# Kernel optimization log

Measured on AMD Instinct MI355X. Metric: run time of the kernel, lower is better.

## Reference

```python
import jax, jax.numpy as jnp
import numpy as np

D_MODEL = 512
D_STATE = 16
D_INNER = 2 * D_MODEL  # expand_factor=2
IN_CH = 256
B_SZ, H_SZ, W_SZ = 4, 32, 32


def setup_inputs() -> dict:
    key = jax.random.key(0)
    ks = jax.random.split(key, 24)
    f = jax.random.normal
    inp = {}
    inp["x_V"] = f(ks[0], (B_SZ, IN_CH, H_SZ, W_SZ), jnp.float32)
    inp["x_I"] = f(ks[1], (B_SZ, IN_CH, H_SZ, W_SZ), jnp.float32)
    # channel_reduce: 1x1 conv + BN (inference stats)
    inp["conv_red_w"] = f(ks[2], (D_MODEL, IN_CH), jnp.float32) * 0.05
    inp["bn_red_g"] = jnp.ones((D_MODEL,), jnp.float32)
    inp["bn_red_b"] = jnp.zeros((D_MODEL,), jnp.float32)
    inp["bn_red_m"] = jnp.zeros((D_MODEL,), jnp.float32)
    inp["bn_red_v"] = jnp.ones((D_MODEL,), jnp.float32)
    # channel_restore: 1x1 conv + BN
    inp["conv_res_w"] = f(ks[3], (IN_CH, D_MODEL), jnp.float32) * 0.05
    inp["bn_res_g"] = jnp.ones((IN_CH,), jnp.float32)
    inp["bn_res_b"] = jnp.zeros((IN_CH,), jnp.float32)
    inp["bn_res_m"] = jnp.zeros((IN_CH,), jnp.float32)
    inp["bn_res_v"] = jnp.ones((IN_CH,), jnp.float32)
    # lambda_predictor convs (1x1 on pooled features == linear)
    inp["lam_w1"] = f(ks[4], (D_MODEL // 4, D_MODEL * 2), jnp.float32) * 0.05
    inp["lam_b1"] = jnp.zeros((D_MODEL // 4,), jnp.float32)
    inp["lam_w2"] = f(ks[5], (2, D_MODEL // 4), jnp.float32) * 0.05
    inp["lam_b2"] = jnp.zeros((2,), jnp.float32)
    # two SimplifiedMamba2Blocks
    for i, p in enumerate(["V", "I"]):
        kk = jax.random.split(ks[6 + i], 6)
        inp[p + "_in_w"] = f(kk[0], (2 * D_INNER, D_MODEL), jnp.float32) * 0.03
        inp[p + "_out_w"] = f(kk[1], (D_MODEL, D_INNER), jnp.float32) * 0.03
        # A = -exp(A_log) in (-1, -0.05): stable decay
        inp[p + "_A_log"] = jnp.log(jax.random.uniform(kk[2], (D_INNER, D_STATE), jnp.float32, 0.05, 0.95))
        inp[p + "_B"] = f(kk[3], (D_INNER, D_STATE), jnp.float32) * 0.05
        inp[p + "_C"] = jnp.full((D_INNER, D_STATE), 0.01, jnp.float32)
        inp[p + "_ln_g"] = jnp.ones((D_MODEL,), jnp.float32)
        inp[p + "_ln_b"] = jnp.zeros((D_MODEL,), jnp.float32)
    inp["gate"] = jnp.asarray(0.1, jnp.float32)
    return inp


def _bn(x, g, b, m, v):
    # x: (B,C,H,W); inference-mode batchnorm
    return (x - m[:, None, None]) / jnp.sqrt(v[:, None, None] + 1e-5) * g[:, None, None] + b[:, None, None]


def _conv1x1(x, w):
    return jnp.einsum('bchw,oc->bohw', x, w)


def _ssm_scan(x_ssm, A, Bm, Cm, reverse):
    # x_ssm: (B,L,I); A,Bm,Cm: (I,S)
    bsz = x_ssm.shape[0]
    h0 = jnp.zeros((bsz, A.shape[0], A.shape[1]), x_ssm.dtype)

    def step(h, xt):  # xt: (B,I)
        h = jnp.clip(h * A + xt[:, :, None] * Bm, -10.0, 10.0)
        return h, jnp.einsum('bis,is->bi', h, Cm)

    _, ys = jax.lax.scan(step, h0, jnp.swapaxes(x_ssm, 0, 1), reverse=reverse)
    return jnp.swapaxes(ys, 0, 1)  # (B,L,I), in original time order


def _mamba(x, ln_g, ln_b, in_w, out_w, A_log, Bm, Cm):
    # LayerNorm
    mu = jnp.mean(x, -1, keepdims=True)
    var = jnp.mean((x - mu) ** 2, -1, keepdims=True)
    xn = (x - mu) / jnp.sqrt(var + 1e-5) * ln_g + ln_b
    xp = xn @ in_w.T  # (B,L,2*I)
    x_ssm, gate = jnp.split(xp, 2, axis=-1)
    A = jnp.clip(-jnp.exp(A_log), -10.0, -0.01)
    yf = _ssm_scan(x_ssm, A, Bm, Cm, False)
    yb = _ssm_scan(x_ssm, A, Bm, Cm, True)
    out = 0.5 * (yf + yb) * jax.nn.silu(gate)
    return out @ out_w.T


def reference(x_V, x_I, conv_red_w, bn_red_g, bn_red_b, bn_red_m, bn_red_v,
              conv_res_w, bn_res_g, bn_res_b, bn_res_m, bn_res_v,
              lam_w1, lam_b1, lam_w2, lam_b2,
              V_in_w, V_out_w, V_A_log, V_B, V_C, V_ln_g, V_ln_b,
              I_in_w, I_out_w, I_A_log, I_B, I_C, I_ln_g, I_ln_b, gate):
    B, _, H, W = x_V.shape
    xVr = jax.nn.relu(_bn(_conv1x1(x_V, conv_red_w), bn_red_g, bn_red_b, bn_red_m, bn_red_v))
    xIr = jax.nn.relu(_bn(_conv1x1(x_I, conv_red_w), bn_red_g, bn_red_b, bn_red_m, bn_red_v))
    # same spatial size -> adaptive pooling and [:B] slicing are identities
    conc = jnp.concatenate([xVr, xIr], axis=1)  # (B, 2*d_model, H, W)

    def lam(c):
        p = jnp.mean(c, axis=(2, 3))  # global avg pool -> (B, 2*d_model)
        h1 = jax.nn.relu(p @ lam_w1.T + lam_b1)
        return jax.nn.softmax(h1 @ lam_w2.T + lam_b2, axis=-1)  # (B,2)

    lamV = lam(conc)
    lamI = lam(conc)

    seq_V = jnp.swapaxes(xVr.reshape(B, D_MODEL, H * W), 1, 2)  # (B,L,D)
    seq_I = jnp.swapaxes(xIr.reshape(B, D_MODEL, H * W), 1, 2)

    outV_std = _mamba(seq_V, V_ln_g, V_ln_b, V_in_w, V_out_w, V_A_log, V_B, V_C)
    outI_std = _mamba(seq_I, I_ln_g, I_ln_b, I_in_w, I_out_w, I_A_log, I_B, I_C)
    outV_cross = _mamba(seq_V, V_ln_g, V_ln_b, V_in_w, V_out_w, V_A_log, jax.lax.stop_gradient(I_B), V_C)
    outI_cross = _mamba(seq_I, I_ln_g, I_ln_b, I_in_w, I_out_w, I_A_log, jax.lax.stop_gradient(V_B), I_C)

    outV = lamV[:, 0][:, None, None] * outV_std + lamV[:, 1][:, None, None] * outV_cross
    outI = lamI[:, 0][:, None, None] * outI_std + lamI[:, 1][:, None, None] * outI_cross

    featV = jnp.swapaxes(outV, 1, 2).reshape(B, D_MODEL, H, W)
    featI = jnp.swapaxes(outI, 1, 2).reshape(B, D_MODEL, H, W)
    featV = _bn(_conv1x1(featV, conv_res_w), bn_res_g, bn_res_b, bn_res_m, bn_res_v)
    featI = _bn(_conv1x1(featI, conv_res_w), bn_res_g, bn_res_b, bn_res_m, bn_res_v)

    g = jax.nn.sigmoid(gate)
    return (x_V + g * featV, x_I + g * featI)
```

## Files before the change

### kernel.cpp

```cpp
#include <hip/hip_runtime.h>
#include <hip/hip_bf16.h>
#include <math.h>

#define L_SZ 1024
#define DM   512
#define DI   1024
#define NS   16
#define CH   256

typedef float4 f4;
typedef __attribute__((ext_vector_type(8))) short short8;
typedef __attribute__((ext_vector_type(8))) unsigned short u16x8;
typedef __attribute__((ext_vector_type(4))) float f32x4;

__device__ __forceinline__ float bf2f(ushort u) {
    union { unsigned int i; float f; } x; x.i = ((unsigned int)u) << 16; return x.f;
}
__device__ __forceinline__ ushort f2bf(float f) {
    union { float f; unsigned int i; } x; x.f = f;
    unsigned int r = x.i + 0x7FFFu + ((x.i >> 16) & 1u);
    return (ushort)(r >> 16);
}
__device__ __forceinline__ uint pkbf(float a, float b) {
    union { __hip_bfloat162 h; uint u; } c;
    c.h = __float22bfloat162_rn(make_float2(a, b));
    return c.u;
}

#define GLOAD16(gp, lp) \
  __builtin_amdgcn_global_load_lds((const __attribute__((address_space(1))) void*)(gp), \
                                   (__attribute__((address_space(3))) void*)(lp), 16, 0, 0)

__global__ __launch_bounds__(256) void k_prep(
    const float* __restrict__ s0, const float* __restrict__ s1,
    const float* __restrict__ s2, const float* __restrict__ s3,
    const float* __restrict__ s4, const float* __restrict__ s5,
    ushort* __restrict__ d0, ushort* __restrict__ d1,
    ushort* __restrict__ d2, ushort* __restrict__ d3,
    ushort* __restrict__ d4, ushort* __restrict__ d5,
    const float* __restrict__ xv, const float* __restrict__ xi,
    ushort* __restrict__ xtv, ushort* __restrict__ xti,
    float* __restrict__ p, unsigned int* __restrict__ cnt)
{
    __shared__ float tile[32][36];
    const int bid = blockIdx.x;
    const int t = threadIdx.x;
    if (bid < 3328) {
        const float* s; ushort* d; int rel;
        if      (bid < 128)  { s = s0; d = d0; rel = bid; }
        else if (bid < 256)  { s = s1; d = d1; rel = bid - 128; }
        else if (bid < 1280) { s = s2; d = d2; rel = bid - 256; }
        else if (bid < 2304) { s = s3; d = d3; rel = bid - 1280; }
        else if (bid < 2816) { s = s4; d = d4; rel = bid - 2304; }
        else                 { s = s5; d = d5; rel = bid - 2816; }
        const int i = rel * 256 + t;
        f4 v = ((const f4*)s)[i];
        ushort4 o;
        o.x = f2bf(v.x); o.y = f2bf(v.y); o.z = f2bf(v.z); o.w = f2bf(v.w);
        ((ushort4*)d)[i] = o;
        return;
    }
    if (bid < 5376) {
        const int rel = bid - 3328;
        const int l0 = (rel & 31) * 32, c0 = ((rel >> 5) & 7) * 32;
        const int z = rel >> 8;
        const int b = z & 3, st = z >> 2;
        const float* x = st ? xi : xv;
        ushort* xt = st ? xti : xtv;
        {
            int cc = t >> 3, ll4 = (t & 7) << 2;
            f4 v = *(const f4*)(x + ((size_t)(b * CH + c0 + cc)) * L_SZ + l0 + ll4);
            tile[cc][ll4 + 0] = v.x; tile[cc][ll4 + 1] = v.y;
            tile[cc][ll4 + 2] = v.z; tile[cc][ll4 + 3] = v.w;
        }
        __syncthreads();
        {
            int ll = t >> 3, cc4 = (t & 7) << 2;
            ushort4 o;
            o.x = f2bf(tile[cc4 + 0][ll]); o.y = f2bf(tile[cc4 + 1][ll]);
            o.z = f2bf(tile[cc4 + 2][ll]); o.w = f2bf(tile[cc4 + 3][ll]);
            *(ushort4*)(xt + ((size_t)(b * L_SZ + l0 + ll)) * CH + c0 + cc4) = o;
        }
        return;
    }
    const f4 z4 = {0.f, 0.f, 0.f, 0.f};
    ((f4*)p)[t]       = z4;
    ((f4*)p)[t + 256] = z4;
    ((f4*)p)[t + 512] = z4;
    ((f4*)p)[t + 768] = z4;
    if (t == 0) *cnt = 0u;
}

template<int MODE, int BM, int BN>
__global__ __launch_bounds__(256) void k_gemm(
    const ushort* __restrict__ A0, const ushort* __restrict__ A1,
    const ushort* __restrict__ B0, const ushort* __restrict__ B1,
    int K,
    float* __restrict__ o0, float* __restrict__ o1,
    ushort* __restrict__ ob0, ushort* __restrict__ ob1,
    ushort* __restrict__ sb0, ushort* __restrict__ sb1,
    const float* __restrict__ pg, const float* __restrict__ pb,
    const float* __restrict__ pm, const float* __restrict__ pv,
    const float* __restrict__ x0, const float* __restrict__ x1,
    const float* __restrict__ gate, float* __restrict__ pp)
{
    constexpr int MT   = BM / 32;
    constexpr int NT   = BN / 32;
    constexpr int ASEG = BM / 16;
    constexpr int NSEG = (BM + BN) / 16;
    constexpr int SPW  = NSEG / 4;
    __shared__ __align__(16) ushort Sl[(BM + BN) * 32];
    const int t = threadIdx.x;
    const int wv = t >> 6, lane = t & 63;
    const int n0 = blockIdx.x * BN, m0 = blockIdx.y * BM;
    const int st = blockIdx.z;
    const ushort* Ap = st ? A1 : A0;
    const ushort* Bp = st ? B1 : B0;
    const int wm = wv >> 1, wn = wv & 1;
    const int lrow = lane & 15, q = lane >> 4;
    f32x4 acc[MT][NT];
    #pragma unroll
    for (int a_ = 0; a_ < MT; ++a_)
        #pragma unroll
        for (int b_ = 0; b_ < NT; ++b_)
            acc[a_][b_] = (f32x4){0.f, 0.f, 0.f, 0.f};
    const int srow = lane >> 2;
    const int skk  = (((lane & 3) ^ ((lane >> 3) & 3)) << 3);
    const int koff = ((q ^ ((lrow >> 1) & 3)) << 3);
    for (int k0 = 0; k0 < K; k0 += 32) {
        #pragma unroll
        for (int s2 = 0; s2 < SPW; ++s2) {
            const int seg = wv * SPW + s2;
            const int grow = (seg < ASEG) ? (m0 + seg * 16 + srow)
                                          : (n0 + (seg - ASEG) * 16 + srow);
            const ushort* src = (seg < ASEG) ? Ap : Bp;
            GLOAD16(src + (size_t)grow * K + k0 + skk, &Sl[seg * 512]);
        }
        __syncthreads();
        short8 af[MT], bfr[NT];
        #pragma unroll
        for (int mt = 0; mt < MT; ++mt)
            af[mt] = *(const short8*)&Sl[(wm * (MT * 16) + mt * 16 + lrow) * 32 + koff];
        #pragma unroll
        for (int nt = 0; nt < NT; ++nt)
            bfr[nt] = *(const short8*)&Sl[(BM + wn * (NT * 16) + nt * 16 + lrow) * 32 + koff];
        #pragma unroll
        for (int mt = 0; mt < MT; ++mt)
            #pragma unroll
            for (int nt = 0; nt < NT; ++nt)
                acc[mt][nt] = __builtin_amdgcn_mfma_f32_16x16x32_bf16(af[mt], bfr[nt], acc[mt][nt], 0, 0, 0);
        __syncthreads();
    }
    if (MODE == 0) {
        ushort* sq = st ? ob1 : ob0;
        const int b = m0 >> 10;
        #pragma unroll
        for (int nt = 0; nt < NT; ++nt) {
            const int gn = n0 + wn * (NT * 16) + nt * 16 + lrow;
            const float s  = pg[gn] * rsqrtf(pv[gn] + 1e-5f);
            const float sh = pb[gn] - pm[gn] * s;
            float psum = 0.f;
            #pragma unroll
            for (int mt = 0; mt < MT; ++mt) {
                const int gm = m0 + wm * (MT * 16) + mt * 16 + q * 4;
                float v[4];
                #pragma unroll
                for (int r = 0; r < 4; ++r) {
                    v[r] = fmaxf(fmaf(acc[mt][nt][r], s, sh), 0.f);
                    psum += v[r];
                }
                const uint u01 = pkbf(v[0], v[1]);
                const uint u23 = pkbf(v[2], v[3]);
                ushort* bp = sq + (size_t)gm * DM + gn;
                bp[0]      = (ushort)u01;
                bp[DM]     = (ushort)(u01 >> 16);
                bp[2 * DM] = (ushort)u23;
                bp[3 * DM] = (ushort)(u23 >> 16);
            }
            psum += __shfl_xor(psum, 16, 64);
            psum += __shfl_xor(psum, 32, 64);
            if (q == 0)
                atomicAdd(pp + (b * 1024 + st * 512 + gn), psum * (1.0f / 1024.0f));
        }
    } else if (MODE == 1) {
        const bool isx = (n0 < 1024);
        ushort* xp = st ? ob1 : ob0;
        ushort* sp = st ? sb1 : sb0;
        #pragma unroll
        for (int nt = 0; nt < NT; ++nt) {
            const int gn = n0 + wn * (NT * 16) + nt * 16 + lrow;
            #pragma unroll
            for (int mt = 0; mt < MT; ++mt) {
                const int gm = m0 + wm * (MT * 16) + mt * 16 + q * 4;
                if (isx) {
                    const uint u01 = pkbf(acc[mt][nt][0], acc[mt][nt][1]);
                    const uint u23 = pkbf(acc[mt][nt][2], acc[mt][nt][3]);
                    ushort* bp = xp + (size_t)gm * DI + gn;
                    bp[0]      = (ushort)u01;
                    bp[DI]     = (ushort)(u01 >> 16);
                    bp[2 * DI] = (ushort)u23;
                    bp[3 * DI] = (ushort)(u23 >> 16);
                } else {
                    float sv[4];
                    #pragma unroll
                    for (int r = 0; r < 4; ++r) {
                        const float v = acc[mt][nt][r];
                        sv[r] = v / (1.f + __expf(-v));
                    }
                    const uint u01 = pkbf(sv[0], sv[1]);
                    const uint u23 = pkbf(sv[2], sv[3]);
                    ushort* bp = sp + (size_t)gm * DI + gn - 1024;
                    bp[0]      = (ushort)u01;
                    bp[DI]     = (ushort)(u01 >> 16);
                    bp[2 * DI] = (ushort)u23;
                    bp[3 * DI] = (ushort)(u23 >> 16);
                }
            }
        }
    } else if (MODE == 2) {
        ushort* fp_ = st ? ob1 : ob0;
        #pragma unroll
        for (int nt = 0; nt < NT; ++nt) {
            const int gn = n0 + wn * (NT * 16) + nt * 16 + lrow;
            #pragma unroll
            for (int mt = 0; mt < MT; ++mt) {
                const int gm = m0 + wm * (MT * 16) + mt * 16 + q * 4;
                const uint u01 = pkbf(acc[mt][nt][0], acc[mt][nt][1]);
                const uint u23 = pkbf(acc[mt][nt][2], acc[mt][nt][3]);
                ushort* bp = fp_ + (size_t)gm * DM + gn;
                bp[0]      = (ushort)u01;
                bp[DM]     = (ushort)(u01 >> 16);
                bp[2 * DM] = (ushort)u23;
                bp[3 * DM] = (ushort)(u23 >> 16);
            }
        }
    } else {
        const float* xin = st ? x1 : x0;
        float* op = st ? o1 : o0;
        const float g = 1.f / (1.f + __expf(-gate[0]));
        #pragma unroll
        for (int nt = 0; nt < NT; ++nt) {
            const int gn = n0 + wn * (NT * 16) + nt * 16 + lrow;
            const float s  = pg[gn] * rsqrtf(pv[gn] + 1e-5f);
            const float sh = pb[gn] - pm[gn] * s;
            #pragma unroll
            for (int mt = 0; mt < MT; ++mt) {
                const int gmb = m0 + wm * (MT * 16) + mt * 16 + q * 4;
                const int b = gmb >> 10, l = gmb & 1023;
                const size_t off = ((size_t)(b * CH + gn)) * L_SZ + l;
                f4 xi = *(const f4*)(xin + off);
                f4 o;
                o.x = xi.x + g * fmaf(acc[mt][nt][0], s, sh);
                o.y = xi.y + g * fmaf(acc[mt][nt][1], s, sh);
                o.z = xi.z + g * fmaf(acc[mt][nt][2], s, sh);
                o.w = xi.w + g * fmaf(acc[mt][nt][3], s, sh);
                *(f4*)(op + off) = o;
            }
        }
    }
}

__global__ __launch_bounds__(256) void k_lam(
    const float* __restrict__ p, const float* __restrict__ w1,
    const float* __restrict__ b1, const float* __restrict__ w2,
    const float* __restrict__ b2, float* __restrict__ h1,
    float* __restrict__ lam, unsigned int* __restrict__ cnt)
{
    __shared__ float lsm[8];
    __shared__ unsigned int tick;
    const int t = threadIdx.x, lane = t & 63, wv = t >> 6;
    const int idx = blockIdx.x * 4 + wv;
    const int b = idx >> 7, j = idx & 127;
    const float* pb = p + b * 1024;
    const float* wr = w1 + j * 1024;
    float s = 0.f;
    #pragma unroll
    for (int k = 0; k < 16; ++k)
        s = fmaf(pb[lane + k * 64], wr[lane + k * 64], s);
    #pragma unroll
    for (int off = 1; off < 64; off <<= 1) s += __shfl_xor(s, off, 64);
    if (lane == 0) h1[idx] = fmaxf(s + b1[j], 0.f);
    __threadfence();
    __syncthreads();
    if (t == 0) tick = atomicAdd(cnt, 1u);
    __syncthreads();
    if (tick != 127u) return;
    __threadfence();
    {
        const int g32 = t >> 5, l32 = t & 31;
        const int bb = g32 >> 1, kk = g32 & 1;
        const float* hb = h1 + bb * 128;
        const float* wr2 = w2 + kk * 128;
        float ss = 0.f;
        #pragma unroll
        for (int u = 0; u < 4; ++u)
            ss = fmaf(hb[l32 + u * 32], wr2[l32 + u * 32], ss);
        #pragma unroll
        for (int off = 1; off < 32; off <<= 1) ss += __shfl_xor(ss, off, 64);
        if (l32 == 0) lsm[g32] = ss + b2[kk];
    }
    __syncthreads();
    if (t < 4) {
        const float a0 = lsm[t * 2], a1 = lsm[t * 2 + 1];
        const float m  = fmaxf(a0, a1);
        const float e0 = __expf(a0 - m), e1 = __expf(a1 - m);
        const float inv = 1.f / (e0 + e1);
        lam[t * 2 + 0] = e0 * inv;
        lam[t * 2 + 1] = e1 * inv;
    }
}

__global__ __launch_bounds__(256) void k_ln(
    const ushort* __restrict__ seq0, const ushort* __restrict__ seq1,
    const float* __restrict__ g0, const float* __restrict__ b0,
    const float* __restrict__ g1, const float* __restrict__ b1,
    ushort* __restrict__ ln0, ushort* __restrict__ ln1)
{
    const int t = threadIdx.x, lane = t & 63, wv = t >> 6;
    const int row = blockIdx.x * 4 + wv, st = blockIdx.y;
    const ushort* seq = st ? seq1 : seq0;
    const float* gg  = st ? g1 : g0;
    const float* bb  = st ? b1 : b0;
    ushort* ln = st ? ln1 : ln0;
    const u16x8 v = *(const u16x8*)(seq + (size_t)row * DM + lane * 8);
    float f[8];
    float s = 0.f, ss = 0.f;
    #pragma unroll
    for (int i = 0; i < 8; ++i) {
        f[i] = bf2f(v[i]);
        s += f[i];
        ss = fmaf(f[i], f[i], ss);
    }
    #pragma unroll
    for (int off = 1; off < 64; off <<= 1) {
        s += __shfl_xor(s, off, 64); ss += __shfl_xor(ss, off, 64);
    }
    const float mu = s * (1.f / 512.f);
    const float rstd = rsqrtf(ss * (1.f / 512.f) - mu * mu + 1e-5f);
    const f4 gv0 = *(const f4*)(gg + lane * 8);
    const f4 gv1 = *(const f4*)(gg + lane * 8 + 4);
    const f4 bv0 = *(const f4*)(bb + lane * 8);
    const f4 bv1 = *(const f4*)(bb + lane * 8 + 4);
    const float gvv[8] = {gv0.x, gv0.y, gv0.z, gv0.w, gv1.x, gv1.y, gv1.z, gv1.w};
    const float bvv[8] = {bv0.x, bv0.y, bv0.z, bv0.w, bv1.x, bv1.y, bv1.z, bv1.w};
    u16x8 o;
    #pragma unroll
    for (int i = 0; i < 8; i += 2) {
        const uint u = pkbf(fmaf((f[i]     - mu) * rstd, gvv[i],     bvv[i]),
                            fmaf((f[i + 1] - mu) * rstd, gvv[i + 1], bvv[i + 1]));
        o[i]     = (ushort)u;
        o[i + 1] = (ushort)(u >> 16);
    }
    *(u16x8*)(ln + (size_t)row * DM + lane * 8) = o;
}

__global__ __launch_bounds__(256) void k_scan(
    const ushort* __restrict__ xsV, const ushort* __restrict__ xsI,
    const float* __restrict__ VA, const float* __restrict__ VB,
    const float* __restrict__ VC, const float* __restrict__ IA,
    const float* __restrict__ IB, const float* __restrict__ IC,
    const float* __restrict__ lam,
    ushort* __restrict__ accfV, ushort* __restrict__ accbV,
    ushort* __restrict__ accfI, ushort* __restrict__ accbI)
{
    __shared__ __align__(16) ushort xbuf[2][32][128];
    const int t = threadIdx.x;
    const int lane = t & 63, wv = t >> 6;
    const int shalf = t & 1;
    const int il = t >> 1;
    const int b = blockIdx.y;
    const int cfg = blockIdx.z & 3, j = blockIdx.z >> 2;
    const int st = cfg >> 1, dir = cfg & 1;
    const ushort* xs = st ? xsI : xsV;
    const float* Alog = st ? IA : VA;
    const float* Cm   = st ? IC : VC;
    const float* Bown = st ? IB : VB;
    const float* Both = st ? VB : IB;
    ushort* out = st ? (dir ? accbI : accfI) : (dir ? accbV : accfV);
    const float lam0 = lam[b * 2 + 0], lam1 = lam[b * 2 + 1];
    float a[8], w[8], g[8];
    const int base = (blockIdx.x * 128 + il) * NS + shalf * 8;
    #pragma unroll
    for (int s = 0; s < 8; ++s) {
        a[s] = fminf(fmaxf(-__expf(Alog[base + s]), -10.f), -0.01f);
        w[s] = 0.5f * Cm[base + s] * fmaf(lam0, Bown[base + s], lam1 * Both[base + s]);
        g[s] = 0.f;
    }
    const ushort* xbase = xs + (size_t)b * L_SZ * DI + blockIdx.x * 128;
    ushort* op = out + (size_t)b * L_SZ * DI + blockIdx.x * 128 + il;
    const int c0    = j == 0 ? 0 : 4 * j - 3;
    const int ncha  = j == 0 ? 4 : 7;
    const int nwarm = j == 0 ? 0 : 3;
    const int lrow  = wv * 4 + (lane >> 4);
    const int lcol8 = (lane & 15) << 3;
    {
        #pragma unroll
        for (int is = 0; is < 2; ++is) {
            const int lr = (c0 << 5) + is * 16 + lrow;
            const int l  = dir ? (1023 - lr) : lr;
            GLOAD16(xbase + (size_t)l * DI + lcol8, &xbuf[0][is * 16 + wv * 4][0]);
        }
    }
    __syncthreads();
    for (int ci = 0; ci < ncha; ++ci) {
        const int cidx = c0 + ci;
        const int buf = ci & 1;
        if (ci + 1 < ncha) {
            #pragma unroll
            for (int is = 0; is < 2; ++is) {
                const int lr = ((cidx + 1) << 5) + is * 16 + lrow;
                const int l  = dir ? (1023 - lr) : lr;
                GLOAD16(xbase + (size_t)l * DI + lcol8, &xbuf[buf ^ 1][is * 16 + wv * 4][0]);
            }
        }
        if (ci < nwarm) {
            #pragma unroll
            for (int n = 0; n < 32; ++n) {
                const float x = bf2f(xbuf[buf][n][il]);
                #pragma unroll
                for (int s = 0; s < 8; ++s)
                    g[s] = fmaf(a[s], g[s], x);
            }
        } else {
            #pragma unroll
            for (int n = 0; n < 32; ++n) {
                const float x = bf2f(xbuf[buf][n][il]);
                float y0 = 0.f, y1 = 0.f;
                #pragma unroll
                for (int s = 0; s < 8; s += 2) {
                    g[s]     = fmaf(a[s],     g[s],     x);
                    y0       = fmaf(g[s],     w[s],     y0);
                    g[s + 1] = fmaf(a[s + 1], g[s + 1], x);
                    y1       = fmaf(g[s + 1], w[s + 1], y1);
                }
                float z = y0 + y1;
                z += __shfl_xor(z, 1, 64);
                if (shalf == 0) {
                    const int lp = (cidx << 5) + n;
                    const int l  = dir ? (1023 - lp) : lp;
                    op[(size_t)l * DI] = f2bf(z);
                }
            }
        }
        __syncthreads();
    }
}

__global__ __launch_bounds__(256) void k_combine(
    const ushort* __restrict__ fV, const ushort* __restrict__ bV,
    const ushort* __restrict__ fI, const ushort* __restrict__ bI,
    const ushort* __restrict__ sgV, const ushort* __restrict__ sgI,
    ushort* __restrict__ yV, ushort* __restrict__ yI)
{
    const int st = blockIdx.y;
    const size_t i = (size_t)blockIdx.x * 256 + threadIdx.x;
    const ushort4 f = ((const ushort4*)(st ? fI : fV))[i];
    const ushort4 g = ((const ushort4*)(st ? bI : bV))[i];
    const ushort4 s = ((const ushort4*)(st ? sgI : sgV))[i];
    ushort4 o;
    o.x = f2bf((bf2f(f.x) + bf2f(g.x)) * bf2f(s.x));
    o.y = f2bf((bf2f(f.y) + bf2f(g.y)) * bf2f(s.y));
    o.z = f2bf((bf2f(f.z) + bf2f(g.z)) * bf2f(s.z));
    o.w = f2bf((bf2f(f.w) + bf2f(g.w)) * bf2f(s.w));
    ((ushort4*)(st ? yI : yV))[i] = o;
}

extern "C" void kernel_launch(void* const* d_in, const int* in_sizes, int n_in,
                              void* d_out, int out_size, void* d_ws, size_t ws_size,
                              hipStream_t stream)
{
    const float* xV       = (const float*)d_in[0];
    const float* xI       = (const float*)d_in[1];
    const float* convredw = (const float*)d_in[2];
    const float* bnredg   = (const float*)d_in[3];
    const float* bnredb   = (const float*)d_in[4];
    const float* bnredm   = (const float*)d_in[5];
    const float* bnredv   = (const float*)d_in[6];
    const float* convresw = (const float*)d_in[7];
    const float* bnresg   = (const float*)d_in[8];
    const float* bnresb   = (const float*)d_in[9];
    const float* bnresm   = (const float*)d_in[10];
    const float* bnresv   = (const float*)d_in[11];
    const float* lamw1    = (const float*)d_in[12];
    const float* lamb1    = (const float*)d_in[13];
    const float* lamw2    = (const float*)d_in[14];
    const float* lamb2    = (const float*)d_in[15];
    const float* Vinw     = (const float*)d_in[16];
    const float* Voutw    = (const float*)d_in[17];
    const float* VAlog    = (const float*)d_in[18];
    const float* VB       = (const float*)d_in[19];
    const float* VC       = (const float*)d_in[20];
    const float* Vlng     = (const float*)d_in[21];
    const float* Vlnb     = (const float*)d_in[22];
    const float* Iinw     = (const float*)d_in[23];
    const float* Ioutw    = (const float*)d_in[24];
    const float* IAlog    = (const float*)d_in[25];
    const float* IB       = (const float*)d_in[26];
    const float* IC       = (const float*)d_in[27];
    const float* Ilng     = (const float*)d_in[28];
    const float* Ilnb     = (const float*)d_in[29];
    const float* gate     = (const float*)d_in[30];

    char* W = (char*)d_ws;
    const size_t MB = 1048576;
    ushort* seqV  = (ushort*)(W + 0);
    ushort* seqI  = (ushort*)(W + 4  * MB);
    float*  p     = (float*)(W + 8 * MB);
    float*  lam   = (float*)(W + 8 * MB + 16384);
    float*  h1    = (float*)(W + 8 * MB + 32768);
    unsigned int* cnt = (unsigned int*)(W + 8 * MB + 49152);
    ushort* sgV   = (ushort*)(W + 17 * MB);
    ushort* sgI   = (ushort*)(W + 25 * MB);
    ushort* accfV = (ushort*)(W + 33 * MB);
    ushort* accbV = (ushort*)(W + 41 * MB);
    ushort* accfI = (ushort*)(W + 49 * MB);
    ushort* accbI = (ushort*)(W + 57 * MB);
    ushort* wred  = (ushort*)(W + 65 * MB);
    ushort* wres  = (ushort*)(W + 65 * MB + 262144);
    ushort* winV  = (ushort*)(W + 66 * MB);
    ushort* winI  = (ushort*)(W + 68 * MB);
    ushort* woutV = (ushort*)(W + 70 * MB);
    ushort* woutI = (ushort*)(W + 71 * MB);
    ushort* xtV   = (ushort*)(W + 72 * MB);
    ushort* xtI   = (ushort*)(W + 74 * MB);
    ushort* lnV   = (ushort*)(W + 76 * MB);
    ushort* lnI   = (ushort*)(W + 80 * MB);
    ushort* xsV   = (ushort*)(W + 84 * MB);
    ushort* xsI   = (ushort*)(W + 92 * MB);
    ushort* yV    = xsV;
    ushort* yI    = xsI;
    ushort* featV = seqV;
    ushort* featI = seqI;
    float*  outp  = (float*)d_out;

    k_prep<<<dim3(5377), 256, 0, stream>>>(
        convredw, convresw, Vinw, Iinw, Voutw, Ioutw,
        wred, wres, winV, winI, woutV, woutI,
        xV, xI, xtV, xtI, p, cnt);
    k_gemm<0, 128, 64><<<dim3(8, 32, 2), 256, 0, stream>>>(xtV, xtI, wred, wred, 256,
        nullptr, nullptr, seqV, seqI, nullptr, nullptr,
        bnredg, bnredb, bnredm, bnredv, nullptr, nullptr, nullptr, p);
    k_lam<<<128, 256, 0, stream>>>(p, lamw1, lamb1, lamw2, lamb2, h1, lam, cnt);
    k_ln<<<dim3(1024, 2), 256, 0, stream>>>(seqV, seqI, Vlng, Vlnb, Ilng, Ilnb, lnV, lnI);
    k_gemm<1, 128, 128><<<dim3(16, 32, 2), 256, 0, stream>>>(lnV, lnI, winV, winI, 512,
        nullptr, nullptr, xsV, xsI, sgV, sgI,
        nullptr, nullptr, nullptr, nullptr, nullptr, nullptr, nullptr, nullptr);
    k_scan<<<dim3(8, 4, 32), 256, 0, stream>>>(xsV, xsI, VAlog, VB, VC,
        IAlog, IB, IC, lam, accfV, accbV, accfI, accbI);
    k_combine<<<dim3(4096, 2), 256, 0, stream>>>(accfV, accbV, accfI, accbI,
        sgV, sgI, yV, yI);
    k_gemm<2, 128, 64><<<dim3(8, 32, 2), 256, 0, stream>>>(yV, yI, woutV, woutI, 1024,
        nullptr, nullptr, featV, featI, nullptr, nullptr,
        nullptr, nullptr, nullptr, nullptr, nullptr, nullptr, nullptr, nullptr);
    k_gemm<3, 64, 64><<<dim3(4, 64, 2), 256, 0, stream>>>(featV, featI, wres, wres, 512,
        outp, outp + 1048576, nullptr, nullptr, nullptr, nullptr,
        bnresg, bnresb, bnresm, bnresv, xV, xI, gate, nullptr);
}
```

Before: 268.1 us.

## Fuse forward/backward scans and gating combine into a single scan kernel

Each scan block now runs the forward and backward recurrences together over a 128-row window with 64-row warm-up halos. It exchanges the partial outputs through shared memory and applies the silu-gate multiply directly, which removes the separate combine kernel and the four bf16 accumulator buffers. This cuts global traffic and one launch, and it halves the block count while doubling per-thread work and shared memory (about 64KB per block), which may reduce occupancy. The final writes are scalar strided stores plus gate loads per element.

```diff
diff --git a/kernel.cpp b/kernel.cpp
--- a/kernel.cpp
+++ b/kernel.cpp
@@ -356,113 +356,133 @@
 
 __global__ __launch_bounds__(256) void k_scan(
     const ushort* __restrict__ xsV, const ushort* __restrict__ xsI,
+    const ushort* __restrict__ sgV, const ushort* __restrict__ sgI,
     const float* __restrict__ VA, const float* __restrict__ VB,
     const float* __restrict__ VC, const float* __restrict__ IA,
     const float* __restrict__ IB, const float* __restrict__ IC,
     const float* __restrict__ lam,
-    ushort* __restrict__ accfV, ushort* __restrict__ accbV,
-    ushort* __restrict__ accfI, ushort* __restrict__ accbI)
+    ushort* __restrict__ yV, ushort* __restrict__ yI)
 {
-    __shared__ __align__(16) ushort xbuf[2][32][128];
+    __shared__ __align__(16) ushort xf[2][32][128];
+    __shared__ __align__(16) ushort xb[2][32][128];
+    __shared__ ushort yfb[64][128];
+    __shared__ ushort ybb[64][128];
     const int t = threadIdx.x;
     const int lane = t & 63, wv = t >> 6;
     const int shalf = t & 1;
     const int il = t >> 1;
     const int b = blockIdx.y;
-    const int cfg = blockIdx.z & 3, j = blockIdx.z >> 2;
-    const int st = cfg >> 1, dir = cfg & 1;
-    const ushort* xs = st ? xsI : xsV;
+    const int st = blockIdx.z >> 3, j = blockIdx.z & 7;
+    const ushort* xrow  = (st ? xsI : xsV) + (size_t)b * L_SZ * DI + blockIdx.x * 128;
+    const ushort* sgrow = (st ? sgI : sgV) + (size_t)b * L_SZ * DI + blockIdx.x * 128;
+    ushort* yrow        = (st ? yI  : yV ) + (size_t)b * L_SZ * DI + blockIdx.x * 128;
     const float* Alog = st ? IA : VA;
     const float* Cm   = st ? IC : VC;
     const float* Bown = st ? IB : VB;
     const float* Both = st ? VB : IB;
-    ushort* out = st ? (dir ? accbI : accfI) : (dir ? accbV : accfV);
     const float lam0 = lam[b * 2 + 0], lam1 = lam[b * 2 + 1];
-    float a[8], w[8], g[8];
+    float a[8], w[8], gf[8], gb[8];
     const int base = (blockIdx.x * 128 + il) * NS + shalf * 8;
     #pragma unroll
     for (int s = 0; s < 8; ++s) {
         a[s] = fminf(fmaxf(-__expf(Alog[base + s]), -10.f), -0.01f);
         w[s] = 0.5f * Cm[base + s] * fmaf(lam0, Bown[base + s], lam1 * Both[base + s]);
-        g[s] = 0.f;
-    }
-    const ushort* xbase = xs + (size_t)b * L_SZ * DI + blockIdx.x * 128;
-    ushort* op = out + (size_t)b * L_SZ * DI + blockIdx.x * 128 + il;
-    const int c0    = j == 0 ? 0 : 4 * j - 3;
-    const int ncha  = j == 0 ? 4 : 7;
-    const int nwarm = j == 0 ? 0 : 3;
-    const int lrow  = wv * 4 + (lane >> 4);
-    const int lcol8 = (lane & 15) << 3;
-    {
-        #pragma unroll
-        for (int is = 0; is < 2; ++is) {
-            const int lr = (c0 << 5) + is * 16 + lrow;
-            const int l  = dir ? (1023 - lr) : lr;
-            GLOAD16(xbase + (size_t)l * DI + lcol8, &xbuf[0][is * 16 + wv * 4][0]);
-        }
+        gf[s] = 0.f; gb[s] = 0.f;
+    }
+    const int row0 = j << 7;
+    const int lr16 = wv * 4 + (lane >> 4);
+    const int lc8  = (lane & 15) << 3;
+    #pragma unroll
+    for (int is = 0; is < 2; ++is) {
+        const int idx = is * 16 + lr16;
+        int rf = row0 - 64 + idx;
+        rf = max(0, min(1023, rf));
+        GLOAD16(xrow + (size_t)rf * DI + lc8, &xf[0][is * 16 + wv * 4][0]);
+        int rb = row0 + 191 - idx;
+        rb = max(0, min(1023, rb));
+        GLOAD16(xrow + (size_t)rb * DI + lc8, &xb[0][is * 16 + wv * 4][0]);
     }
     __syncthreads();
-    for (int ci = 0; ci < ncha; ++ci) {
-        const int cidx = c0 + ci;
-        const int buf = ci & 1;
-        if (ci + 1 < ncha) {
+    for (int si = 0; si < 6; ++si) {
+        const int buf = si & 1;
+        if (si < 5) {
             #pragma unroll
             for (int is = 0; is < 2; ++is) {
-                const int lr = ((cidx + 1) << 5) + is * 16 + lrow;
-                const int l  = dir ? (1023 - lr) : lr;
-                GLOAD16(xbase + (size_t)l * DI + lcol8, &xbuf[buf ^ 1][is * 16 + wv * 4][0]);
-            }
-        }
-        if (ci < nwarm) {
+                const int idx = is * 16 + lr16;
+                int rf = row0 - 64 + (si + 1) * 32 + idx;
+                rf = max(0, min(1023, rf));
+                GLOAD16(xrow + (size_t)rf * DI + lc8, &xf[buf ^ 1][is * 16 + wv * 4][0]);
+                int rb = row0 + 191 - (si + 1) * 32 - idx;
+                rb = max(0, min(1023, rb));
+                GLOAD16(xrow + (size_t)rb * DI + lc8, &xb[buf ^ 1][is * 16 + wv * 4][0]);
+            }
+        }
+        if (si == 2) {
+            if (j == 0) for (int s = 0; s < 8; ++s) gf[s] = 0.f;
+            if (j == 7) for (int s = 0; s < 8; ++s) gb[s] = 0.f;
+        }
+        if (si < 2) {
             #pragma unroll
             for (int n = 0; n < 32; ++n) {
-                const float x = bf2f(xbuf[buf][n][il]);
+                const float vf = bf2f(xf[buf][n][il]);
+                const float vb = bf2f(xb[buf][n][il]);
                 #pragma unroll
-                for (int s = 0; s < 8; ++s)
-                    g[s] = fmaf(a[s], g[s], x);
+                for (int s = 0; s < 8; ++s) {
+                    gf[s] = fmaf(a[s], gf[s], vf);
+                    gb[s] = fmaf(a[s], gb[s], vb);
+                }
+            }
+        } else if (si < 4) {
+            const int nb = (si - 2) * 32;
+            #pragma unroll
+            for (int n = 0; n < 32; ++n) {
+                const float vf = bf2f(xf[buf][n][il]);
+                const float vb = bf2f(xb[buf][n][il]);
+                float yf = 0.f, yb = 0.f;
+                #pragma unroll
+                for (int s = 0; s < 8; ++s) {
+                    gf[s] = fmaf(a[s], gf[s], vf);
+                    yf    = fmaf(gf[s], w[s], yf);
+                    gb[s] = fmaf(a[s], gb[s], vb);
+                    yb    = fmaf(gb[s], w[s], yb);
+                }
+                yf += __shfl_xor(yf, 1, 64);
+                yb += __shfl_xor(yb, 1, 64);
+                if (shalf == 0) {
+                    yfb[nb + n][il]      = f2bf(yf);
+                    ybb[63 - nb - n][il] = f2bf(yb);
+                }
             }
         } else {
+            const int nb = (si - 4) * 32;
             #pragma unroll
             for (int n = 0; n < 32; ++n) {
-                const float x = bf2f(xbuf[buf][n][il]);
-                float y0 = 0.f, y1 = 0.f;
+                const float vf = bf2f(xf[buf][n][il]);
+                const float vb = bf2f(xb[buf][n][il]);
+                float yf = 0.f, yb = 0.f;
                 #pragma unroll
-                for (int s = 0; s < 8; s += 2) {
-                    g[s]     = fmaf(a[s],     g[s],     x);
-                    y0       = fmaf(g[s],     w[s],     y0);
-                    g[s + 1] = fmaf(a[s + 1], g[s + 1], x);
-                    y1       = fmaf(g[s + 1], w[s + 1], y1);
-                }
-                float z = y0 + y1;
-                z += __shfl_xor(z, 1, 64);
+                for (int s = 0; s < 8; ++s) {
+                    gf[s] = fmaf(a[s], gf[s], vf);
+                    yf    = fmaf(gf[s], w[s], yf);
+                    gb[s] = fmaf(a[s], gb[s], vb);
+                    yb    = fmaf(gb[s], w[s], yb);
+                }
+                yf += __shfl_xor(yf, 1, 64);
+                yb += __shfl_xor(yb, 1, 64);
                 if (shalf == 0) {
-                    const int lp = (cidx << 5) + n;
-                    const int l  = dir ? (1023 - lp) : lp;
-                    op[(size_t)l * DI] = f2bf(z);
+                    const int nf_ = 64 + nb + n;
+                    const float zf = (yf + bf2f(ybb[nb + n][il]))
+                                   * bf2f(sgrow[(size_t)(row0 + nf_) * DI + il]);
+                    yrow[(size_t)(row0 + nf_) * DI + il] = f2bf(zf);
+                    const int rb_ = 63 - nb - n;
+                    const float zb = (yb + bf2f(yfb[rb_][il]))
+                                   * bf2f(sgrow[(size_t)(row0 + rb_) * DI + il]);
+                    yrow[(size_t)(row0 + rb_) * DI + il] = f2bf(zb);
                 }
             }
         }
         __syncthreads();
     }
-}
-
-__global__ __launch_bounds__(256) void k_combine(
-    const ushort* __restrict__ fV, const ushort* __restrict__ bV,
-    const ushort* __restrict__ fI, const ushort* __restrict__ bI,
-    const ushort* __restrict__ sgV, const ushort* __restrict__ sgI,
-    ushort* __restrict__ yV, ushort* __restrict__ yI)
-{
-    const int st = blockIdx.y;
-    const size_t i = (size_t)blockIdx.x * 256 + threadIdx.x;
-    const ushort4 f = ((const ushort4*)(st ? fI : fV))[i];
-    const ushort4 g = ((const ushort4*)(st ? bI : bV))[i];
-    const ushort4 s = ((const ushort4*)(st ? sgI : sgV))[i];
-    ushort4 o;
-    o.x = f2bf((bf2f(f.x) + bf2f(g.x)) * bf2f(s.x));
-    o.y = f2bf((bf2f(f.y) + bf2f(g.y)) * bf2f(s.y));
-    o.z = f2bf((bf2f(f.z) + bf2f(g.z)) * bf2f(s.z));
-    o.w = f2bf((bf2f(f.w) + bf2f(g.w)) * bf2f(s.w));
-    ((ushort4*)(st ? yI : yV))[i] = o;
 }
 
 extern "C" void kernel_launch(void* const* d_in, const int* in_sizes, int n_in,
@@ -511,10 +531,8 @@
     unsigned int* cnt = (unsigned int*)(W + 8 * MB + 49152);
     ushort* sgV   = (ushort*)(W + 17 * MB);
     ushort* sgI   = (ushort*)(W + 25 * MB);
-    ushort* accfV = (ushort*)(W + 33 * MB);
-    ushort* accbV = (ushort*)(W + 41 * MB);
-    ushort* accfI = (ushort*)(W + 49 * MB);
-    ushort* accbI = (ushort*)(W + 57 * MB);
+    ushort* yV    = (ushort*)(W + 33 * MB);
+    ushort* yI    = (ushort*)(W + 41 * MB);
     ushort* wred  = (ushort*)(W + 65 * MB);
     ushort* wres  = (ushort*)(W + 65 * MB + 262144);
     ushort* winV  = (ushort*)(W + 66 * MB);
@@ -527,8 +545,6 @@
     ushort* lnI   = (ushort*)(W + 80 * MB);
     ushort* xsV   = (ushort*)(W + 84 * MB);
     ushort* xsI   = (ushort*)(W + 92 * MB);
-    ushort* yV    = xsV;
-    ushort* yI    = xsI;
     ushort* featV = seqV;
     ushort* featI = seqI;
     float*  outp  = (float*)d_out;
@@ -545,10 +561,8 @@
     k_gemm<1, 128, 128><<<dim3(16, 32, 2), 256, 0, stream>>>(lnV, lnI, winV, winI, 512,
         nullptr, nullptr, xsV, xsI, sgV, sgI,
         nullptr, nullptr, nullptr, nullptr, nullptr, nullptr, nullptr, nullptr);
-    k_scan<<<dim3(8, 4, 32), 256, 0, stream>>>(xsV, xsI, VAlog, VB, VC,
-        IAlog, IB, IC, lam, accfV, accbV, accfI, accbI);
-    k_combine<<<dim3(4096, 2), 256, 0, stream>>>(accfV, accbV, accfI, accbI,
-        sgV, sgI, yV, yI);
+    k_scan<<<dim3(8, 4, 16), 256, 0, stream>>>(xsV, xsI, sgV, sgI,
+        VAlog, VB, VC, IAlog, IB, IC, lam, yV, yI);
     k_gemm<2, 128, 64><<<dim3(8, 32, 2), 256, 0, stream>>>(yV, yI, woutV, woutI, 1024,
         nullptr, nullptr, featV, featI, nullptr, nullptr,
         nullptr, nullptr, nullptr, nullptr, nullptr, nullptr, nullptr, nullptr);
```

Measured after the change: 270.1 us. No clear change (+0.7%).
